# Performance work log

Measured on AMD Instinct MI355X. Metric: run time of the kernel, lower is better.

Reference implementation:

```python
import jax, jax.numpy as jnp
import numpy as np

B, S, IN, H, OUT, P = 4096, 200, 8, 128, 8, 50


def setup_inputs() -> dict:
    key = jax.random.key(0)
    ks = jax.random.split(key, 9)
    s_in = 1.0 / np.sqrt(IN)
    s_h = 1.0 / np.sqrt(H)
    return {
        "x": jax.random.normal(ks[0], (B, S, IN), dtype=jnp.float32),
        "Win": jax.random.uniform(ks[1], (H, IN), jnp.float32, -s_in, s_in),
        "bin_": jax.random.uniform(ks[2], (H,), jnp.float32, -s_in, s_in),
        "W1": jax.random.uniform(ks[3], (H, H), jnp.float32, -s_h, s_h),
        "b1": jax.random.uniform(ks[4], (H,), jnp.float32, -s_h, s_h),
        "W2": jax.random.uniform(ks[5], (H, H), jnp.float32, -s_h, s_h),
        "b2": jax.random.uniform(ks[6], (H,), jnp.float32, -s_h, s_h),
        "Wout": jax.random.uniform(ks[7], (OUT, H), jnp.float32, -s_h, s_h),
        "bout": jax.random.uniform(ks[8], (OUT,), jnp.float32, -s_h, s_h),
    }


def reference(x, Win, bin_, W1, b1, W2, b2, Wout, bout):
    # input layer applied to all tokens: [B,S,IN] -> [B,S,H]
    h = jnp.einsum("bsi,hi->bsh", x, Win) + bin_
    h0 = h[:, -1, :]  # ODE initial state [B,H]

    def ode_f(y):  # autonomous Linear-Tanh-Linear vector field
        return jnp.tanh(y @ W1.T + b1) @ W2.T + b2

    dt = jnp.float32(1.0)  # linspace(0, P-1, P) has unit spacing

    def rk4_step(y, _):
        k1 = ode_f(y)
        k2 = ode_f(y + 0.5 * dt * k1)
        k3 = ode_f(y + 0.5 * dt * k2)
        k4 = ode_f(y + dt * k3)
        y_next = y + (dt / 6.0) * (k1 + 2.0 * k2 + 2.0 * k3 + k4)
        return y_next, y_next

    _, traj = jax.lax.scan(rk4_step, h0, None, length=P - 1)  # [P-1,B,H]
    ode_out = jnp.concatenate([h0[None], traj], axis=0)  # [P,B,H]
    ode_out = jnp.transpose(ode_out, (1, 0, 2))  # [B,P,H]
    return jnp.einsum("bph,oh->bpo", ode_out, Wout) + bout
```

## Files before the change

kernel.cpp:

```cpp
#include <hip/hip_runtime.h>

typedef _Float16 f16x8 __attribute__((ext_vector_type(8)));
typedef _Float16 f16x4 __attribute__((ext_vector_type(4)));
typedef float    f32x4 __attribute__((ext_vector_type(4)));

#define MFMA16(A, B, C) __builtin_amdgcn_mfma_f32_16x16x32_f16((A), (B), (C), 0, 0, 0)

constexpr int Bsz = 4096, Ssz = 200, INsz = 8, Hsz = 128, OUTsz = 8, Psz = 50;
constexpr int ROWS = 16;
constexpr int WS_G = 0, WS_GO = 16384, WS_D = 17408, WS_CO = 17536;

__global__ void precomp_kernel(const float* __restrict__ W1, const float* __restrict__ W2,
                               const float* __restrict__ b2, const float* __restrict__ Wout,
                               float* __restrict__ ws) {
  int tid = (int)blockIdx.x * 256 + (int)threadIdx.x;
  if (tid < 16384) {
    int j = tid >> 7, k = tid & 127;
    float acc = 0.f;
    #pragma unroll 8
    for (int m = 0; m < 128; ++m) acc = fmaf(W1[j*128 + m], W2[m*128 + k], acc);
    ws[WS_G + tid] = acc;
  } else if (tid < 16384 + 1024) {
    int t = tid - 16384; int o = t >> 7, k = t & 127;
    float acc = 0.f;
    #pragma unroll 8
    for (int m = 0; m < 128; ++m) acc = fmaf(Wout[o*128 + m], W2[m*128 + k], acc);
    ws[WS_GO + t] = acc;
  } else if (tid < 16384 + 1024 + 128) {
    int j = tid - 17408;
    float acc = 0.f;
    for (int m = 0; m < 128; ++m) acc = fmaf(b2[m], W1[j*128 + m], acc);
    ws[WS_D + j] = acc;
  } else if (tid < 16384 + 1024 + 128 + 8) {
    int o = tid - 17536;
    float acc = 0.f;
    for (int m = 0; m < 128; ++m) acc = fmaf(b2[m], Wout[o*128 + m], acc);
    ws[WS_CO + o] = acc;
  }
}

#define SPLIT8(PTR, HI, LO) do { \
    const f32x4 va_ = *(const f32x4*)(PTR); \
    const f32x4 vb_ = *(const f32x4*)((PTR) + 4); \
    _Pragma("unroll") \
    for (int j_ = 0; j_ < 4; ++j_) { \
      _Float16 h0_ = (_Float16)va_[j_]; \
      (HI)[j_]     = h0_; \
      (LO)[j_]     = (_Float16)(va_[j_] - (float)h0_); \
      _Float16 h1_ = (_Float16)vb_[j_]; \
      (HI)[j_ + 4] = h1_; \
      (LO)[j_ + 4] = (_Float16)(vb_[j_] - (float)h1_); \
    } \
  } while (0)

#define STG(BH, BL, AH, AL, BI, O) do { \
    f32x4 c_ = (BI); \
    f32x4 e_ = {0.f,0.f,0.f,0.f}, f_ = {0.f,0.f,0.f,0.f}; \
    _Pragma("unroll") \
    for (int ks_ = 0; ks_ < 4; ++ks_) { \
      const f16x8 uh_ = *(const f16x8*)(&(BH)[(ks_*64 + l)*8]); \
      const f16x8 ul_ = *(const f16x8*)(&(BL)[(ks_*64 + l)*8]); \
      c_ = MFMA16((AH)[ks_], uh_, c_); \
      e_ = MFMA16((AL)[ks_], uh_, e_); \
      f_ = MFMA16((AH)[ks_], ul_, f_); \
    } \
    (O) = c_ + e_ + f_; \
  } while (0)

#define WPK(DH, DL, V) do { \
    f16x4 wh_, wl_; \
    _Pragma("unroll") \
    for (int q_ = 0; q_ < 4; ++q_) { \
      _Float16 hh_ = (_Float16)(V)[q_]; \
      wh_[q_] = hh_; wl_[q_] = (_Float16)((V)[q_] - (float)hh_); \
    } \
    *(f16x4*)(&(DH)[wb0]) = wh_; \
    *(f16x4*)(&(DL)[wb0]) = wl_; \
  } while (0)

__device__ inline f32x4 tanh4(f32x4 z) {
  f32x4 o;
  #pragma unroll
  for (int q = 0; q < 4; ++q) {
    float zz = fminf(fmaxf(z[q], -15.f), 15.f);
    float e  = __builtin_amdgcn_exp2f(2.8853900817779268f * zz);
    o[q] = (e - 1.f) * __builtin_amdgcn_rcpf(e + 1.f);
  }
  return o;
}

__global__ __launch_bounds__(512, 2) void node_rk4_kernel(
    const float* __restrict__ x,    const float* __restrict__ Win,
    const float* __restrict__ binp, const float* __restrict__ W1,
    const float* __restrict__ b1,   const float* __restrict__ Wout,
    const float* __restrict__ bout, const float* __restrict__ ws,
    float* __restrict__ out)
{
  __shared__ _Float16 bufA_hi[2048], bufA_lo[2048], bufB_hi[2048], bufB_lo[2048];

  const int tid = (int)threadIdx.x;
  const int w   = tid >> 6;
  const int l   = tid & 63;
  const int g   = l >> 4;
  const int r   = l & 15;
  const int rowbase = (int)blockIdx.x * ROWS;
  const int ch0 = w * 16;
  const int wb0 = ((w >> 1)*512 + (2*(w & 1) + (g >> 1))*128 + r*8) + 4*(g & 1);

  f16x8 Gh[4], Gl[4];
  #pragma unroll
  for (int ks = 0; ks < 4; ++ks)
    SPLIT8(ws + WS_G + (size_t)(ch0 + r)*Hsz + 32*ks + 8*g, Gh[ks], Gl[ks]);

  f16x8 goh[4], gol[4];
  #pragma unroll
  for (int ks = 0; ks < 4; ++ks) {
    if (r < OUTsz) SPLIT8(ws + WS_GO + (size_t)r*Hsz + 32*ks + 8*g, goh[ks], gol[ks]);
    else {
      #pragma unroll
      for (int j = 0; j < 8; ++j) { goh[ks][j] = (_Float16)0.f; gol[ks][j] = (_Float16)0.f; }
    }
  }

  const f32x4 dv  = *(const f32x4*)(ws + WS_D + ch0 + 4*g);
  const f32x4 dv6 = 6.f * dv;
  f32x4 cov6, boutv;
  if (g < 2) { cov6 = 6.f * *(const f32x4*)(ws + WS_CO + 4*g);
               boutv = *(const f32x4*)(bout + 4*g); }
  else { cov6 = f32x4{0.f,0.f,0.f,0.f}; boutv = f32x4{0.f,0.f,0.f,0.f}; }

  const float* xr = x + ((size_t)(rowbase + r)*Ssz + (Ssz - 1))*INsz;
  const f32x4 xa = *(const f32x4*)xr;
  const f32x4 xb = *(const f32x4*)(xr + 4);
  f32x4 yv;
  {
    const f32x4 binv = *(const f32x4*)(binp + ch0 + 4*g);
    #pragma unroll
    for (int q = 0; q < 4; ++q) {
      const float* wrp = Win + (size_t)(ch0 + 4*g + q)*INsz;
      const f32x4 wa = *(const f32x4*)wrp;
      const f32x4 wb = *(const f32x4*)(wrp + 4);
      float acc = binv[q];
      #pragma unroll
      for (int i = 0; i < 4; ++i) acc += xa[i]*wa[i] + xb[i]*wb[i];
      yv[q] = acc;
    }
  }

  WPK(bufA_hi, bufA_lo, yv);
  __syncthreads();

  f32x4 z, o;
  {
    f16x8 a1h[4], a1l[4];
    #pragma unroll
    for (int ks = 0; ks < 4; ++ks)
      SPLIT8(W1 + (size_t)(ch0 + r)*Hsz + 32*ks + 8*g, a1h[ks], a1l[ks]);
    const f32x4 b1v = *(const f32x4*)(b1 + ch0 + 4*g);
    STG(bufA_hi, bufA_lo, a1h, a1l, b1v, z);

    if (w == 0) {
      f16x8 woh[4], wol[4];
      #pragma unroll
      for (int ks = 0; ks < 4; ++ks) {
        if (r < OUTsz) SPLIT8(Wout + (size_t)r*Hsz + 32*ks + 8*g, woh[ks], wol[ks]);
        else {
          #pragma unroll
          for (int j = 0; j < 8; ++j) { woh[ks][j] = (_Float16)0.f; wol[ks][j] = (_Float16)0.f; }
        }
      }
      const f32x4 zero = {0.f,0.f,0.f,0.f};
      STG(bufA_hi, bufA_lo, woh, wol, zero, o);
    } else {
      o = f32x4{0.f,0.f,0.f,0.f};
    }
  }
  __syncthreads();

  f32x4 Ta, m, t;
  #pragma unroll 1
  for (int p = 0; p < Psz; ++p) {
    if (w == 0 && g < 2) {
      float* dst = out + ((size_t)(rowbase + r)*Psz + p)*OUTsz + 4*g;
      *(f32x4*)dst = o + boutv;
    }
    if (p == Psz - 1) break;

    t = tanh4(z);
    Ta = t;
    WPK(bufA_hi, bufA_lo, t);
    __syncthreads();

    STG(bufA_hi, bufA_lo, Gh, Gl, dv, m);
    t = tanh4(z + 0.5f*m);
    Ta += 2.f*t;
    WPK(bufB_hi, bufB_lo, t);
    __syncthreads();

    STG(bufB_hi, bufB_lo, Gh, Gl, dv, m);
    t = tanh4(z + 0.5f*m);
    Ta += 2.f*t;
    WPK(bufA_hi, bufA_lo, t);
    __syncthreads();

    STG(bufA_hi, bufA_lo, Gh, Gl, dv, m);
    t = tanh4(z + m);
    Ta += t;
    WPK(bufB_hi, bufB_lo, Ta);
    __syncthreads();

    STG(bufB_hi, bufB_lo, Gh, Gl, dv6, m);
    z += (1.f/6.f)*m;
    if (w == 0) {
      f32x4 mo;
      STG(bufB_hi, bufB_lo, goh, gol, cov6, mo);
      o += (1.f/6.f)*mo;
    }
  }
}

extern "C" void kernel_launch(void* const* d_in, const int* in_sizes, int n_in,
                              void* d_out, int out_size, void* d_ws, size_t ws_size,
                              hipStream_t stream) {
  (void)in_sizes; (void)n_in; (void)ws_size; (void)out_size;
  const float* x    = (const float*)d_in[0];
  const float* Win  = (const float*)d_in[1];
  const float* binp = (const float*)d_in[2];
  const float* W1   = (const float*)d_in[3];
  const float* b1   = (const float*)d_in[4];
  const float* W2   = (const float*)d_in[5];
  const float* b2   = (const float*)d_in[6];
  const float* Wout = (const float*)d_in[7];
  const float* bout = (const float*)d_in[8];
  float* ws = (float*)d_ws;

  precomp_kernel<<<69, 256, 0, stream>>>(W1, W2, b2, Wout, ws);
  node_rk4_kernel<<<Bsz / ROWS, 512, 0, stream>>>(x, Win, binp, W1, b1, Wout,
                                                  bout, ws, (float*)d_out);
}
```

Measured before the change: 105.9 us.

## Split each RK4 matvec across two wave groups with K-split and LDS reduction

```diff
diff --git a/kernel.cpp b/kernel.cpp
--- a/kernel.cpp
+++ b/kernel.cpp
@@ -53,18 +53,37 @@
     } \
   } while (0)
 
-#define STG(BH, BL, AH, AL, BI, O) do { \
-    f32x4 c_ = (BI); \
+#define MPHASE(AH, AL, SH, SL, BIAS, P) do { \
+    const f16x8 u0h_ = *(const f16x8*)(&(SH)[((ks0+0)*64 + l)*8]); \
+    const f16x8 u0l_ = *(const f16x8*)(&(SL)[((ks0+0)*64 + l)*8]); \
+    const f16x8 u1h_ = *(const f16x8*)(&(SH)[((ks0+1)*64 + l)*8]); \
+    const f16x8 u1l_ = *(const f16x8*)(&(SL)[((ks0+1)*64 + l)*8]); \
+    f32x4 c_ = (BIAS); \
     f32x4 e_ = {0.f,0.f,0.f,0.f}, f_ = {0.f,0.f,0.f,0.f}; \
-    _Pragma("unroll") \
-    for (int ks_ = 0; ks_ < 4; ++ks_) { \
-      const f16x8 uh_ = *(const f16x8*)(&(BH)[(ks_*64 + l)*8]); \
-      const f16x8 ul_ = *(const f16x8*)(&(BL)[(ks_*64 + l)*8]); \
-      c_ = MFMA16((AH)[ks_], uh_, c_); \
-      e_ = MFMA16((AL)[ks_], uh_, e_); \
-      f_ = MFMA16((AH)[ks_], ul_, f_); \
-    } \
-    (O) = c_ + e_ + f_; \
+    c_ = MFMA16((AH)[0], u0h_, c_); \
+    e_ = MFMA16((AL)[0], u0h_, e_); \
+    f_ = MFMA16((AH)[0], u0l_, f_); \
+    c_ = MFMA16((AH)[1], u1h_, c_); \
+    e_ = MFMA16((AL)[1], u1h_, e_); \
+    f_ = MFMA16((AH)[1], u1l_, f_); \
+    (P) = c_ + e_ + f_; \
+    if (!owner) pbuf[c][l] = (P); \
+  } while (0)
+
+#define GOPHASE(SH, SL) do { \
+    const int gb_ = 2*c; \
+    const f16x8 v0h_ = *(const f16x8*)(&(SH)[((gb_+0)*64 + l)*8]); \
+    const f16x8 v0l_ = *(const f16x8*)(&(SL)[((gb_+0)*64 + l)*8]); \
+    const f16x8 v1h_ = *(const f16x8*)(&(SH)[((gb_+1)*64 + l)*8]); \
+    const f16x8 v1l_ = *(const f16x8*)(&(SL)[((gb_+1)*64 + l)*8]); \
+    f32x4 cg_ = {0.f,0.f,0.f,0.f}, eg_ = {0.f,0.f,0.f,0.f}, fg_ = {0.f,0.f,0.f,0.f}; \
+    cg_ = MFMA16(goh[0], v0h_, cg_); \
+    eg_ = MFMA16(gol[0], v0h_, eg_); \
+    fg_ = MFMA16(goh[0], v0l_, fg_); \
+    cg_ = MFMA16(goh[1], v1h_, cg_); \
+    eg_ = MFMA16(gol[1], v1h_, eg_); \
+    fg_ = MFMA16(goh[1], v1l_, fg_); \
+    pbuf[8 + c][l] = cg_ + eg_ + fg_; \
   } while (0)
 
 #define WPK(DH, DL, V) do { \
@@ -89,7 +108,7 @@
   return o;
 }
 
-__global__ __launch_bounds__(512, 2) void node_rk4_kernel(
+__global__ __launch_bounds__(1024) void node_rk4_kernel(
     const float* __restrict__ x,    const float* __restrict__ Win,
     const float* __restrict__ binp, const float* __restrict__ W1,
     const float* __restrict__ b1,   const float* __restrict__ Wout,
@@ -97,44 +116,53 @@
     float* __restrict__ out)
 {
   __shared__ _Float16 bufA_hi[2048], bufA_lo[2048], bufB_hi[2048], bufB_lo[2048];
+  __shared__ f32x4 pbuf[10][64];
 
   const int tid = (int)threadIdx.x;
   const int w   = tid >> 6;
+  const int c   = w & 7;
+  const int h   = w >> 3;
+  const bool owner = (h == 0);
   const int l   = tid & 63;
   const int g   = l >> 4;
   const int r   = l & 15;
   const int rowbase = (int)blockIdx.x * ROWS;
-  const int ch0 = w * 16;
-  const int wb0 = ((w >> 1)*512 + (2*(w & 1) + (g >> 1))*128 + r*8) + 4*(g & 1);
-
-  f16x8 Gh[4], Gl[4];
+  const int ch0 = c * 16;
+  const int ks0 = 2 * h;
+  const int wb0 = ((c >> 1)*512 + (2*(c & 1) + (g >> 1))*128 + r*8) + 4*(g & 1);
+  const f32x4 zero = {0.f,0.f,0.f,0.f};
+
+  f16x8 Gh[2], Gl[2];
   #pragma unroll
-  for (int ks = 0; ks < 4; ++ks)
-    SPLIT8(ws + WS_G + (size_t)(ch0 + r)*Hsz + 32*ks + 8*g, Gh[ks], Gl[ks]);
-
-  f16x8 goh[4], gol[4];
-  #pragma unroll
-  for (int ks = 0; ks < 4; ++ks) {
-    if (r < OUTsz) SPLIT8(ws + WS_GO + (size_t)r*Hsz + 32*ks + 8*g, goh[ks], gol[ks]);
-    else {
-      #pragma unroll
-      for (int j = 0; j < 8; ++j) { goh[ks][j] = (_Float16)0.f; gol[ks][j] = (_Float16)0.f; }
-    }
-  }
-
-  const f32x4 dv  = *(const f32x4*)(ws + WS_D + ch0 + 4*g);
-  const f32x4 dv6 = 6.f * dv;
-  f32x4 cov6, boutv;
-  if (g < 2) { cov6 = 6.f * *(const f32x4*)(ws + WS_CO + 4*g);
-               boutv = *(const f32x4*)(bout + 4*g); }
-  else { cov6 = f32x4{0.f,0.f,0.f,0.f}; boutv = f32x4{0.f,0.f,0.f,0.f}; }
-
-  const float* xr = x + ((size_t)(rowbase + r)*Ssz + (Ssz - 1))*INsz;
-  const f32x4 xa = *(const f32x4*)xr;
-  const f32x4 xb = *(const f32x4*)(xr + 4);
-  f32x4 yv;
-  {
+  for (int ks = 0; ks < 2; ++ks)
+    SPLIT8(ws + WS_G + (size_t)(ch0 + r)*Hsz + 32*(ks0 + ks) + 8*g, Gh[ks], Gl[ks]);
+
+  f16x8 goh[2], gol[2];
+  if (!owner && c < 2) {
+    #pragma unroll
+    for (int ks = 0; ks < 2; ++ks) {
+      if (r < OUTsz) SPLIT8(ws + WS_GO + (size_t)r*Hsz + 32*(2*c + ks) + 8*g, goh[ks], gol[ks]);
+      else {
+        #pragma unroll
+        for (int j = 0; j < 8; ++j) { goh[ks][j] = (_Float16)0.f; gol[ks][j] = (_Float16)0.f; }
+      }
+    }
+  }
+
+  const f32x4 dvw  = owner ? *(const f32x4*)(ws + WS_D + ch0 + 4*g) : zero;
+  const f32x4 dv6w = 6.f * dvw;
+  f32x4 cov6 = zero, boutv = zero;
+  if (w == 0 && g < 2) {
+    cov6  = 6.f * *(const f32x4*)(ws + WS_CO + 4*g);
+    boutv = *(const f32x4*)(bout + 4*g);
+  }
+
+  if (owner) {
+    const float* xr = x + ((size_t)(rowbase + r)*Ssz + (Ssz - 1))*INsz;
+    const f32x4 xa = *(const f32x4*)xr;
+    const f32x4 xb = *(const f32x4*)(xr + 4);
     const f32x4 binv = *(const f32x4*)(binp + ch0 + 4*g);
+    f32x4 yv;
     #pragma unroll
     for (int q = 0; q < 4; ++q) {
       const float* wrp = Win + (size_t)(ch0 + 4*g + q)*INsz;
@@ -145,39 +173,43 @@
       for (int i = 0; i < 4; ++i) acc += xa[i]*wa[i] + xb[i]*wb[i];
       yv[q] = acc;
     }
-  }
-
-  WPK(bufA_hi, bufA_lo, yv);
+    WPK(bufA_hi, bufA_lo, yv);
+  }
   __syncthreads();
 
-  f32x4 z, o;
+  f32x4 z, o, Ta, m, pA;
   {
-    f16x8 a1h[4], a1l[4];
+    f16x8 a1h[2], a1l[2];
     #pragma unroll
-    for (int ks = 0; ks < 4; ++ks)
-      SPLIT8(W1 + (size_t)(ch0 + r)*Hsz + 32*ks + 8*g, a1h[ks], a1l[ks]);
-    const f32x4 b1v = *(const f32x4*)(b1 + ch0 + 4*g);
-    STG(bufA_hi, bufA_lo, a1h, a1l, b1v, z);
-
-    if (w == 0) {
-      f16x8 woh[4], wol[4];
+    for (int ks = 0; ks < 2; ++ks)
+      SPLIT8(W1 + (size_t)(ch0 + r)*Hsz + 32*(ks0 + ks) + 8*g, a1h[ks], a1l[ks]);
+    const f32x4 b1w = owner ? *(const f32x4*)(b1 + ch0 + 4*g) : zero;
+    MPHASE(a1h, a1l, bufA_hi, bufA_lo, b1w, pA);
+    if (!owner && c < 2) {
+      f16x8 woh[2], wol[2];
       #pragma unroll
-      for (int ks = 0; ks < 4; ++ks) {
-        if (r < OUTsz) SPLIT8(Wout + (size_t)r*Hsz + 32*ks + 8*g, woh[ks], wol[ks]);
+      for (int ks = 0; ks < 2; ++ks) {
+        if (r < OUTsz) SPLIT8(Wout + (size_t)r*Hsz + 32*(2*c + ks) + 8*g, woh[ks], wol[ks]);
         else {
           #pragma unroll
           for (int j = 0; j < 8; ++j) { woh[ks][j] = (_Float16)0.f; wol[ks][j] = (_Float16)0.f; }
         }
       }
-      const f32x4 zero = {0.f,0.f,0.f,0.f};
-      STG(bufA_hi, bufA_lo, woh, wol, zero, o);
-    } else {
-      o = f32x4{0.f,0.f,0.f,0.f};
-    }
-  }
-  __syncthreads();
-
-  f32x4 Ta, m, t;
+      const int gb = 2*c;
+      const f16x8 v0h = *(const f16x8*)(&bufA_hi[((gb+0)*64 + l)*8]);
+      const f16x8 v0l = *(const f16x8*)(&bufA_lo[((gb+0)*64 + l)*8]);
+      const f16x8 v1h = *(const f16x8*)(&bufA_hi[((gb+1)*64 + l)*8]);
+      const f16x8 v1l = *(const f16x8*)(&bufA_lo[((gb+1)*64 + l)*8]);
+      f32x4 cg = zero, eg = zero, fg = zero;
+      cg = MFMA16(woh[0], v0h, cg); eg = MFMA16(wol[0], v0h, eg); fg = MFMA16(woh[0], v0l, fg);
+      cg = MFMA16(woh[1], v1h, cg); eg = MFMA16(wol[1], v1h, eg); fg = MFMA16(woh[1], v1l, fg);
+      pbuf[8 + c][l] = cg + eg + fg;
+    }
+    __syncthreads();
+    if (owner) z = pA + pbuf[c][l];
+    if (w == 0) o = pbuf[8][l] + pbuf[9][l];
+  }
+
   #pragma unroll 1
   for (int p = 0; p < Psz; ++p) {
     if (w == 0 && g < 2) {
@@ -186,36 +218,32 @@
     }
     if (p == Psz - 1) break;
 
-    t = tanh4(z);
-    Ta = t;
-    WPK(bufA_hi, bufA_lo, t);
-    __syncthreads();
-
-    STG(bufA_hi, bufA_lo, Gh, Gl, dv, m);
-    t = tanh4(z + 0.5f*m);
-    Ta += 2.f*t;
-    WPK(bufB_hi, bufB_lo, t);
-    __syncthreads();
-
-    STG(bufB_hi, bufB_lo, Gh, Gl, dv, m);
-    t = tanh4(z + 0.5f*m);
-    Ta += 2.f*t;
-    WPK(bufA_hi, bufA_lo, t);
-    __syncthreads();
-
-    STG(bufA_hi, bufA_lo, Gh, Gl, dv, m);
-    t = tanh4(z + m);
-    Ta += t;
-    WPK(bufB_hi, bufB_lo, Ta);
-    __syncthreads();
-
-    STG(bufB_hi, bufB_lo, Gh, Gl, dv6, m);
-    z += (1.f/6.f)*m;
-    if (w == 0) {
-      f32x4 mo;
-      STG(bufB_hi, bufB_lo, goh, gol, cov6, mo);
-      o += (1.f/6.f)*mo;
-    }
+    if (owner) { f32x4 t = tanh4(z); Ta = t; WPK(bufA_hi, bufA_lo, t); }
+    __syncthreads();
+
+    MPHASE(Gh, Gl, bufA_hi, bufA_lo, dvw, pA);
+    __syncthreads();
+    if (owner) { m = pA + pbuf[c][l]; f32x4 t = tanh4(z + 0.5f*m);
+                 Ta += 2.f*t; WPK(bufB_hi, bufB_lo, t); }
+    __syncthreads();
+
+    MPHASE(Gh, Gl, bufB_hi, bufB_lo, dvw, pA);
+    __syncthreads();
+    if (owner) { m = pA + pbuf[c][l]; f32x4 t = tanh4(z + 0.5f*m);
+                 Ta += 2.f*t; WPK(bufA_hi, bufA_lo, t); }
+    __syncthreads();
+
+    MPHASE(Gh, Gl, bufA_hi, bufA_lo, dvw, pA);
+    __syncthreads();
+    if (owner) { m = pA + pbuf[c][l]; f32x4 t = tanh4(z + m);
+                 Ta += t; WPK(bufB_hi, bufB_lo, Ta); }
+    __syncthreads();
+
+    MPHASE(Gh, Gl, bufB_hi, bufB_lo, dv6w, pA);
+    if (!owner && c < 2) GOPHASE(bufB_hi, bufB_lo);
+    __syncthreads();
+    if (owner) { m = pA + pbuf[c][l]; z += (1.f/6.f)*m; }
+    if (w == 0) o += (1.f/6.f)*(pbuf[8][l] + pbuf[9][l] + cov6);
   }
 }
 
@@ -235,6 +263,6 @@
   float* ws = (float*)d_ws;
 
   precomp_kernel<<<69, 256, 0, stream>>>(W1, W2, b2, Wout, ws);
-  node_rk4_kernel<<<Bsz / ROWS, 512, 0, stream>>>(x, Win, binp, W1, b1, Wout,
-                                                  bout, ws, (float*)d_out);
-}
+  node_rk4_kernel<<<Bsz / ROWS, 1024, 0, stream>>>(x, Win, binp, W1, b1, Wout,
+                                                   bout, ws, (float*)d_out);
+}
```

Measured after the change: 145.3 us. 1.37x slower.

## Prescale tanh state, split MFMA chains, drop low-precision output MFMAs, fuse output stage

Applied to the files above, without the earlier changes.

```diff
diff --git a/kernel.cpp b/kernel.cpp
--- a/kernel.cpp
+++ b/kernel.cpp
@@ -2,6 +2,7 @@
 
 typedef _Float16 f16x8 __attribute__((ext_vector_type(8)));
 typedef _Float16 f16x4 __attribute__((ext_vector_type(4)));
+typedef __fp16   h16x2 __attribute__((ext_vector_type(2)));
 typedef float    f32x4 __attribute__((ext_vector_type(4)));
 
 #define MFMA16(A, B, C) __builtin_amdgcn_mfma_f32_16x16x32_f16((A), (B), (C), 0, 0, 0)
@@ -9,6 +10,11 @@
 constexpr int Bsz = 4096, Ssz = 200, INsz = 8, Hsz = 128, OUTsz = 8, Psz = 50;
 constexpr int ROWS = 16;
 constexpr int WS_G = 0, WS_GO = 16384, WS_D = 17408, WS_CO = 17536;
+
+#define KF   2.8853900817779268f
+#define KH   1.4426950408889634f
+#define K6   0.4808983469629878f
+#define KCLAMP 43.2808512266689f
 
 __global__ void precomp_kernel(const float* __restrict__ W1, const float* __restrict__ W2,
                                const float* __restrict__ b2, const float* __restrict__ Wout,
@@ -40,52 +46,98 @@
 }
 
 #define SPLIT8(PTR, HI, LO) do { \
-    const f32x4 va_ = *(const f32x4*)(PTR); \
-    const f32x4 vb_ = *(const f32x4*)((PTR) + 4); \
     _Pragma("unroll") \
-    for (int j_ = 0; j_ < 4; ++j_) { \
-      _Float16 h0_ = (_Float16)va_[j_]; \
-      (HI)[j_]     = h0_; \
-      (LO)[j_]     = (_Float16)(va_[j_] - (float)h0_); \
-      _Float16 h1_ = (_Float16)vb_[j_]; \
-      (HI)[j_ + 4] = h1_; \
-      (LO)[j_ + 4] = (_Float16)(vb_[j_] - (float)h1_); \
+    for (int j_ = 0; j_ < 8; ++j_) { \
+      float v_ = (PTR)[j_]; \
+      _Float16 h_ = (_Float16)v_; \
+      (HI)[j_] = h_; \
+      (LO)[j_] = (_Float16)(v_ - (float)h_); \
     } \
   } while (0)
 
+#define SPLIT8H(PTR, HI) do { \
+    _Pragma("unroll") \
+    for (int j_ = 0; j_ < 8; ++j_) (HI)[j_] = (_Float16)(PTR)[j_]; \
+  } while (0)
+
 #define STG(BH, BL, AH, AL, BI, O) do { \
-    f32x4 c_ = (BI); \
-    f32x4 e_ = {0.f,0.f,0.f,0.f}, f_ = {0.f,0.f,0.f,0.f}; \
-    _Pragma("unroll") \
-    for (int ks_ = 0; ks_ < 4; ++ks_) { \
-      const f16x8 uh_ = *(const f16x8*)(&(BH)[(ks_*64 + l)*8]); \
-      const f16x8 ul_ = *(const f16x8*)(&(BL)[(ks_*64 + l)*8]); \
-      c_ = MFMA16((AH)[ks_], uh_, c_); \
-      e_ = MFMA16((AL)[ks_], uh_, e_); \
-      f_ = MFMA16((AH)[ks_], ul_, f_); \
+    const f16x8 uh0_ = *(const f16x8*)(&(BH)[(0*64 + l)*8]); \
+    const f16x8 uh1_ = *(const f16x8*)(&(BH)[(1*64 + l)*8]); \
+    const f16x8 uh2_ = *(const f16x8*)(&(BH)[(2*64 + l)*8]); \
+    const f16x8 uh3_ = *(const f16x8*)(&(BH)[(3*64 + l)*8]); \
+    const f16x8 ul0_ = *(const f16x8*)(&(BL)[(0*64 + l)*8]); \
+    const f16x8 ul1_ = *(const f16x8*)(&(BL)[(1*64 + l)*8]); \
+    const f16x8 ul2_ = *(const f16x8*)(&(BL)[(2*64 + l)*8]); \
+    const f16x8 ul3_ = *(const f16x8*)(&(BL)[(3*64 + l)*8]); \
+    f32x4 cA_ = (BI), cB_ = {0.f,0.f,0.f,0.f}; \
+    f32x4 eA_ = {0.f,0.f,0.f,0.f}, eB_ = {0.f,0.f,0.f,0.f}; \
+    f32x4 fA_ = {0.f,0.f,0.f,0.f}, fB_ = {0.f,0.f,0.f,0.f}; \
+    cA_ = MFMA16((AH)[0], uh0_, cA_);  cB_ = MFMA16((AH)[2], uh2_, cB_); \
+    eA_ = MFMA16((AL)[0], uh0_, eA_);  eB_ = MFMA16((AL)[2], uh2_, eB_); \
+    fA_ = MFMA16((AH)[0], ul0_, fA_);  fB_ = MFMA16((AH)[2], ul2_, fB_); \
+    cA_ = MFMA16((AH)[1], uh1_, cA_);  cB_ = MFMA16((AH)[3], uh3_, cB_); \
+    eA_ = MFMA16((AL)[1], uh1_, eA_);  eB_ = MFMA16((AL)[3], uh3_, eB_); \
+    fA_ = MFMA16((AH)[1], ul1_, fA_);  fB_ = MFMA16((AH)[3], ul3_, fB_); \
+    (O) = ((cA_ + cB_) + (eA_ + eB_)) + (fA_ + fB_); \
+  } while (0)
+
+#define STG5(BH, BL, AH, AL, BI, O, GOH, GOBI, MO) do { \
+    const f16x8 uh0_ = *(const f16x8*)(&(BH)[(0*64 + l)*8]); \
+    const f16x8 uh1_ = *(const f16x8*)(&(BH)[(1*64 + l)*8]); \
+    const f16x8 uh2_ = *(const f16x8*)(&(BH)[(2*64 + l)*8]); \
+    const f16x8 uh3_ = *(const f16x8*)(&(BH)[(3*64 + l)*8]); \
+    const f16x8 ul0_ = *(const f16x8*)(&(BL)[(0*64 + l)*8]); \
+    const f16x8 ul1_ = *(const f16x8*)(&(BL)[(1*64 + l)*8]); \
+    const f16x8 ul2_ = *(const f16x8*)(&(BL)[(2*64 + l)*8]); \
+    const f16x8 ul3_ = *(const f16x8*)(&(BL)[(3*64 + l)*8]); \
+    f32x4 cA_ = (BI), cB_ = {0.f,0.f,0.f,0.f}; \
+    f32x4 eA_ = {0.f,0.f,0.f,0.f}, eB_ = {0.f,0.f,0.f,0.f}; \
+    f32x4 fA_ = {0.f,0.f,0.f,0.f}, fB_ = {0.f,0.f,0.f,0.f}; \
+    cA_ = MFMA16((AH)[0], uh0_, cA_);  cB_ = MFMA16((AH)[2], uh2_, cB_); \
+    eA_ = MFMA16((AL)[0], uh0_, eA_);  eB_ = MFMA16((AL)[2], uh2_, eB_); \
+    fA_ = MFMA16((AH)[0], ul0_, fA_);  fB_ = MFMA16((AH)[2], ul2_, fB_); \
+    cA_ = MFMA16((AH)[1], uh1_, cA_);  cB_ = MFMA16((AH)[3], uh3_, cB_); \
+    eA_ = MFMA16((AL)[1], uh1_, eA_);  eB_ = MFMA16((AL)[3], uh3_, eB_); \
+    fA_ = MFMA16((AH)[1], ul1_, fA_);  fB_ = MFMA16((AH)[3], ul3_, fB_); \
+    (O) = ((cA_ + cB_) + (eA_ + eB_)) + (fA_ + fB_); \
+    if (w == 0) { \
+      f32x4 gA_ = (GOBI), gB_ = {0.f,0.f,0.f,0.f}; \
+      gA_ = MFMA16((GOH)[0], uh0_, gA_);  gB_ = MFMA16((GOH)[2], uh2_, gB_); \
+      gA_ = MFMA16((GOH)[1], uh1_, gA_);  gB_ = MFMA16((GOH)[3], uh3_, gB_); \
+      (MO) = gA_ + gB_; \
     } \
-    (O) = c_ + e_ + f_; \
   } while (0)
 
 #define WPK(DH, DL, V) do { \
+    h16x2 h0_ = __builtin_amdgcn_cvt_pkrtz((V)[0], (V)[1]); \
+    h16x2 h1_ = __builtin_amdgcn_cvt_pkrtz((V)[2], (V)[3]); \
+    h16x2 l0_ = __builtin_amdgcn_cvt_pkrtz((V)[0] - (float)h0_[0], (V)[1] - (float)h0_[1]); \
+    h16x2 l1_ = __builtin_amdgcn_cvt_pkrtz((V)[2] - (float)h1_[0], (V)[3] - (float)h1_[1]); \
     f16x4 wh_, wl_; \
-    _Pragma("unroll") \
-    for (int q_ = 0; q_ < 4; ++q_) { \
-      _Float16 hh_ = (_Float16)(V)[q_]; \
-      wh_[q_] = hh_; wl_[q_] = (_Float16)((V)[q_] - (float)hh_); \
-    } \
+    wh_[0] = (_Float16)h0_[0]; wh_[1] = (_Float16)h0_[1]; \
+    wh_[2] = (_Float16)h1_[0]; wh_[3] = (_Float16)h1_[1]; \
+    wl_[0] = (_Float16)l0_[0]; wl_[1] = (_Float16)l0_[1]; \
+    wl_[2] = (_Float16)l1_[0]; wl_[3] = (_Float16)l1_[1]; \
     *(f16x4*)(&(DH)[wb0]) = wh_; \
     *(f16x4*)(&(DL)[wb0]) = wl_; \
   } while (0)
 
-__device__ inline f32x4 tanh4(f32x4 z) {
+__device__ inline f32x4 tanhK4(f32x4 zz) {
   f32x4 o;
   #pragma unroll
   for (int q = 0; q < 4; ++q) {
-    float zz = fminf(fmaxf(z[q], -15.f), 15.f);
-    float e  = __builtin_amdgcn_exp2f(2.8853900817779268f * zz);
-    o[q] = (e - 1.f) * __builtin_amdgcn_rcpf(e + 1.f);
-  }
+    float a = __builtin_amdgcn_fmed3f(zz[q], -KCLAMP, KCLAMP);
+    float e = __builtin_amdgcn_exp2f(a);
+    float r = __builtin_amdgcn_rcpf(e + 1.f);
+    o[q] = fmaf(-2.f, r, 1.f);
+  }
+  return o;
+}
+
+__device__ inline f32x4 fma4(float s, f32x4 a, f32x4 b) {
+  f32x4 o;
+  #pragma unroll
+  for (int q = 0; q < 4; ++q) o[q] = fmaf(s, a[q], b[q]);
   return o;
 }
 
@@ -106,28 +158,30 @@
   const int rowbase = (int)blockIdx.x * ROWS;
   const int ch0 = w * 16;
   const int wb0 = ((w >> 1)*512 + (2*(w & 1) + (g >> 1))*128 + r*8) + 4*(g & 1);
+  const f32x4 zero = {0.f,0.f,0.f,0.f};
 
   f16x8 Gh[4], Gl[4];
   #pragma unroll
   for (int ks = 0; ks < 4; ++ks)
     SPLIT8(ws + WS_G + (size_t)(ch0 + r)*Hsz + 32*ks + 8*g, Gh[ks], Gl[ks]);
 
-  f16x8 goh[4], gol[4];
+  f16x8 goh[4];
   #pragma unroll
   for (int ks = 0; ks < 4; ++ks) {
-    if (r < OUTsz) SPLIT8(ws + WS_GO + (size_t)r*Hsz + 32*ks + 8*g, goh[ks], gol[ks]);
+    if (r < OUTsz) SPLIT8H(ws + WS_GO + (size_t)r*Hsz + 32*ks + 8*g, goh[ks]);
     else {
       #pragma unroll
-      for (int j = 0; j < 8; ++j) { goh[ks][j] = (_Float16)0.f; gol[ks][j] = (_Float16)0.f; }
+      for (int j = 0; j < 8; ++j) goh[ks][j] = (_Float16)0.f;
     }
   }
 
   const f32x4 dv  = *(const f32x4*)(ws + WS_D + ch0 + 4*g);
   const f32x4 dv6 = 6.f * dv;
-  f32x4 cov6, boutv;
-  if (g < 2) { cov6 = 6.f * *(const f32x4*)(ws + WS_CO + 4*g);
-               boutv = *(const f32x4*)(bout + 4*g); }
-  else { cov6 = f32x4{0.f,0.f,0.f,0.f}; boutv = f32x4{0.f,0.f,0.f,0.f}; }
+  f32x4 cov6 = zero, boutv = zero;
+  if (w == 0 && g < 2) {
+    cov6  = 6.f * *(const f32x4*)(ws + WS_CO + 4*g);
+    boutv = *(const f32x4*)(bout + 4*g);
+  }
 
   const float* xr = x + ((size_t)(rowbase + r)*Ssz + (Ssz - 1))*INsz;
   const f32x4 xa = *(const f32x4*)xr;
@@ -150,34 +204,30 @@
   WPK(bufA_hi, bufA_lo, yv);
   __syncthreads();
 
-  f32x4 z, o;
+  f32x4 zK, o = zero;
   {
     f16x8 a1h[4], a1l[4];
     #pragma unroll
     for (int ks = 0; ks < 4; ++ks)
       SPLIT8(W1 + (size_t)(ch0 + r)*Hsz + 32*ks + 8*g, a1h[ks], a1l[ks]);
+    f16x8 woh[4];
+    #pragma unroll
+    for (int ks = 0; ks < 4; ++ks) {
+      if (w == 0 && r < OUTsz) SPLIT8H(Wout + (size_t)r*Hsz + 32*ks + 8*g, woh[ks]);
+      else {
+        #pragma unroll
+        for (int j = 0; j < 8; ++j) woh[ks][j] = (_Float16)0.f;
+      }
+    }
     const f32x4 b1v = *(const f32x4*)(b1 + ch0 + 4*g);
-    STG(bufA_hi, bufA_lo, a1h, a1l, b1v, z);
-
-    if (w == 0) {
-      f16x8 woh[4], wol[4];
-      #pragma unroll
-      for (int ks = 0; ks < 4; ++ks) {
-        if (r < OUTsz) SPLIT8(Wout + (size_t)r*Hsz + 32*ks + 8*g, woh[ks], wol[ks]);
-        else {
-          #pragma unroll
-          for (int j = 0; j < 8; ++j) { woh[ks][j] = (_Float16)0.f; wol[ks][j] = (_Float16)0.f; }
-        }
-      }
-      const f32x4 zero = {0.f,0.f,0.f,0.f};
-      STG(bufA_hi, bufA_lo, woh, wol, zero, o);
-    } else {
-      o = f32x4{0.f,0.f,0.f,0.f};
-    }
+    f32x4 z, mo = zero;
+    STG5(bufA_hi, bufA_lo, a1h, a1l, b1v, z, woh, zero, mo);
+    zK = KF * z;
+    if (w == 0) o = mo;
   }
   __syncthreads();
 
-  f32x4 Ta, m, t;
+  f32x4 Ta, m, t, mo;
   #pragma unroll 1
   for (int p = 0; p < Psz; ++p) {
     if (w == 0 && g < 2) {
@@ -186,36 +236,32 @@
     }
     if (p == Psz - 1) break;
 
-    t = tanh4(z);
+    t = tanhK4(zK);
+    WPK(bufA_hi, bufA_lo, t);
+    __syncthreads();
     Ta = t;
+
+    STG(bufA_hi, bufA_lo, Gh, Gl, dv, m);
+    t = tanhK4(fma4(KH, m, zK));
+    WPK(bufB_hi, bufB_lo, t);
+    __syncthreads();
+    Ta = Ta + 2.f*t;
+
+    STG(bufB_hi, bufB_lo, Gh, Gl, dv, m);
+    t = tanhK4(fma4(KH, m, zK));
     WPK(bufA_hi, bufA_lo, t);
     __syncthreads();
+    Ta = Ta + 2.f*t;
 
     STG(bufA_hi, bufA_lo, Gh, Gl, dv, m);
-    t = tanh4(z + 0.5f*m);
-    Ta += 2.f*t;
-    WPK(bufB_hi, bufB_lo, t);
-    __syncthreads();
-
-    STG(bufB_hi, bufB_lo, Gh, Gl, dv, m);
-    t = tanh4(z + 0.5f*m);
-    Ta += 2.f*t;
-    WPK(bufA_hi, bufA_lo, t);
-    __syncthreads();
-
-    STG(bufA_hi, bufA_lo, Gh, Gl, dv, m);
-    t = tanh4(z + m);
-    Ta += t;
+    t = tanhK4(fma4(KF, m, zK));
+    Ta = Ta + t;
     WPK(bufB_hi, bufB_lo, Ta);
     __syncthreads();
 
-    STG(bufB_hi, bufB_lo, Gh, Gl, dv6, m);
-    z += (1.f/6.f)*m;
-    if (w == 0) {
-      f32x4 mo;
-      STG(bufB_hi, bufB_lo, goh, gol, cov6, mo);
-      o += (1.f/6.f)*mo;
-    }
+    STG5(bufB_hi, bufB_lo, Gh, Gl, dv6, m, goh, cov6, mo);
+    zK = fma4(K6, m, zK);
+    if (w == 0) o = o + (1.f/6.f)*mo;
   }
 }
 
```

Result: slower. 110.7 us (+4.6%).
